# Kernel tuning notes

Measured on AMD Instinct MI355X. Metric: run time of the kernel, lower is better.

Reference implementation:

```python
import jax, jax.numpy as jnp
import numpy as np
import math

DIM = 1024
N_HEADS = 16
HEAD_DIM = DIM // N_HEADS
MAX_LEN = 4096
THETA = 10000.0
LN_EPS = 1e-5


def _rope_tables(dim, max_len, theta=THETA):
    # matches precompute_rope: freqs over even indices, angles = outer(t, freqs)
    inv = 1.0 / theta ** (np.arange(0, dim, 2, dtype=np.float32) / dim)
    t = np.arange(max_len, dtype=np.float32)
    ang = np.outer(t, inv)  # [max_len, dim//2]
    return jnp.asarray(np.cos(ang)), jnp.asarray(np.sin(ang))


def setup_inputs() -> dict:
    key = jax.random.key(0)
    ks = jax.random.split(key, 5)
    B, T, D = 2, 2048, DIM
    s = 1.0 / math.sqrt(D)
    x = jax.random.normal(ks[0], (B, T, D), dtype=jnp.float32)
    wq = jax.random.normal(ks[1], (D, D), dtype=jnp.float32) * s
    wk = jax.random.normal(ks[2], (D, D), dtype=jnp.float32) * s
    wv = jax.random.normal(ks[3], (D, D), dtype=jnp.float32) * s
    wo = jax.random.normal(ks[4], (D, D), dtype=jnp.float32) * s
    ln_g = jnp.ones((D,), dtype=jnp.float32)
    ln_b = jnp.zeros((D,), dtype=jnp.float32)
    cos, sin = _rope_tables(HEAD_DIM, MAX_LEN)
    return {"x": x, "wq": wq, "wk": wk, "wv": wv, "wo": wo,
            "ln_g": ln_g, "ln_b": ln_b, "cos": cos, "sin": sin}


def _rotate(x, cos, sin):
    # x: [B, T, H, hd]; complex multiply on interleaved (even, odd) pairs
    B, T, H, hd = x.shape
    xr = x.reshape(B, T, H, hd // 2, 2)
    x0, x1 = xr[..., 0], xr[..., 1]
    c = cos[None, :T, None, :]
    s = sin[None, :T, None, :]
    o0 = x0 * c - x1 * s
    o1 = x0 * s + x1 * c
    return jnp.stack([o0, o1], axis=-1).reshape(B, T, H, hd)


def reference(x, wq, wk, wv, wo, ln_g, ln_b, cos, sin):
    B, T, D = x.shape
    H, hd = N_HEADS, HEAD_DIM
    # LayerNorm
    mu = jnp.mean(x, axis=-1, keepdims=True)
    var = jnp.var(x, axis=-1, keepdims=True)
    h = (x - mu) * jax.lax.rsqrt(var + LN_EPS) * ln_g + ln_b
    # QKV projections (torch Linear: h @ W.T)
    q = jnp.einsum('btd,ed->bte', h, wq).reshape(B, T, H, hd)
    k = jnp.einsum('btd,ed->bte', h, wk).reshape(B, T, H, hd)
    v = jnp.einsum('btd,ed->bte', h, wv).reshape(B, T, H, hd)
    q = _rotate(q, cos, sin)
    k = _rotate(k, cos, sin)
    # full (non-causal) attention, scores [B, H, T, T]
    scores = jnp.einsum('bqhd,bkhd->bhqk', q, k) / math.sqrt(hd)
    attn = jax.nn.softmax(scores, axis=-1)
    out = jnp.einsum('bhqk,bkhd->bqhd', attn, v).reshape(B, T, D)
    return jnp.einsum('btd,ed->bte', out, wo)
```

## Files before the change

kernel.cpp:

```cpp
#include <hip/hip_runtime.h>
#include <hip/hip_bf16.h>

typedef __attribute__((ext_vector_type(4))) float          fx4;
typedef __attribute__((ext_vector_type(8))) __bf16         bfx8;
typedef __attribute__((ext_vector_type(8))) unsigned short usx8;
typedef __attribute__((ext_vector_type(4))) unsigned short usx4;

#define TLEN 2048
#define ROWS 4096
#define D    1024

__device__ __forceinline__ float bf2f(unsigned short u) {
    union { unsigned int i; float f; } v; v.i = ((unsigned int)u) << 16; return v.f;
}
__device__ __forceinline__ unsigned short f2bf(float f) {
    union { float f; unsigned int i; } v; v.f = f;
    unsigned int r = v.i + 0x7fffu + ((v.i >> 16) & 1u);
    return (unsigned short)(r >> 16);
}
__device__ __forceinline__ unsigned int cvtpk_bf16(float lo, float hi) {
    unsigned int r;
    asm("v_cvt_pk_bf16_f32 %0, %1, %2" : "=v"(r) : "v"(lo), "v"(hi));
    return r;
}
__device__ __forceinline__ float fast_cos(float a) {
    float r; asm("v_cos_f32 %0, %1" : "=v"(r) : "v"(a)); return r;
}
__device__ __forceinline__ float fast_sin(float a) {
    float r; asm("v_sin_f32 %0, %1" : "=v"(r) : "v"(a)); return r;
}
__device__ __forceinline__ void gload_lds16(const unsigned short* g, unsigned short* l) {
    __builtin_amdgcn_global_load_lds((const __attribute__((address_space(1))) void*)g,
                                     (__attribute__((address_space(3))) void*)l, 16, 0, 0);
}

__device__ __forceinline__ usx4 cvt4(fx4 a) {
    usx4 o;
    #pragma unroll
    for (int j = 0; j < 4; j++) o[j] = f2bf(a[j]);
    return o;
}
__global__ __launch_bounds__(256) void prep_kernel(const float* __restrict__ x,
                                                   const float* __restrict__ g,
                                                   const float* __restrict__ bta,
                                                   const float* __restrict__ wq, const float* __restrict__ wk,
                                                   const float* __restrict__ wv, const float* __restrict__ wo,
                                                   unsigned short* __restrict__ hout,
                                                   unsigned short* __restrict__ wqkv,
                                                   unsigned short* __restrict__ wob) {
    const int tid = threadIdx.x;
    if (blockIdx.x >= 4096) {
        const int i = (blockIdx.x - 4096) * 256 + tid;
        ((usx4*)wqkv)[i]          = cvt4(((const fx4*)wq)[i]);
        ((usx4*)wqkv)[262144 + i] = cvt4(((const fx4*)wk)[i]);
        ((usx4*)wqkv)[524288 + i] = cvt4(((const fx4*)wv)[i]);
        ((usx4*)wob)[i]           = cvt4(((const fx4*)wo)[i]);
        return;
    }
    const int row = blockIdx.x;
    fx4 v = ((const fx4*)(x + (size_t)row * D))[tid];
    float s  = v[0] + v[1] + v[2] + v[3];
    float s2 = v[0]*v[0] + v[1]*v[1] + v[2]*v[2] + v[3]*v[3];
    #pragma unroll
    for (int mk = 32; mk >= 1; mk >>= 1) { s += __shfl_xor(s, mk); s2 += __shfl_xor(s2, mk); }
    __shared__ float red[8];
    const int wave = tid >> 6, lane = tid & 63;
    if (lane == 0) { red[wave] = s; red[4 + wave] = s2; }
    __syncthreads();
    s  = red[0] + red[1] + red[2] + red[3];
    s2 = red[4] + red[5] + red[6] + red[7];
    float mu   = s * (1.0f / D);
    float var  = s2 * (1.0f / D) - mu * mu;
    float rstd = rsqrtf(var + 1e-5f);
    fx4 gv = ((const fx4*)g)[tid];
    fx4 bv = ((const fx4*)bta)[tid];
    usx4 o;
    #pragma unroll
    for (int j = 0; j < 4; j++) o[j] = f2bf((v[j] - mu) * rstd * gv[j] + bv[j]);
    ((usx4*)hout)[(size_t)row * 256 + tid] = o;
}

__global__ __launch_bounds__(256) void qkvt_gemm(const unsigned short* __restrict__ hbuf,
                                                 const unsigned short* __restrict__ wqkv,
                                                 unsigned short* __restrict__ qkout,
                                                 unsigned short* __restrict__ vtout) {
    constexpr int K = 1024;
    __shared__ __align__(16) unsigned short As[128 * 64];
    __shared__ __align__(16) unsigned short Bs[128 * 64];
    const int tid = threadIdx.x, lane = tid & 63, wave = tid >> 6;
    const int fr = lane & 15, fq = lane >> 4;
    const int wr = wave >> 1, wc = wave & 1;

    const int id = blockIdx.x;
    const bool isqk = id < 512;
    int bm, bn;
    const unsigned short *Ab, *Bb;
    if (isqk) {
        bm = id & 31; bn = id >> 5;
        Ab = hbuf + (size_t)(bm * 128) * K;
        Bb = wqkv + (size_t)(bn * 128) * K;
    } else {
        int j = id - 512; bm = j & 7; bn = j >> 3;
        Ab = wqkv + (size_t)(2048 * 1024) + (size_t)(bm * 128) * K;
        Bb = hbuf + (size_t)(bn * 128) * K;
    }

    const int srow   = wave * 8 + (lane >> 3);
    const int sc_dst = (lane & 7) * 8;
    const int sc_src = ((lane & 7) ^ (lane >> 3)) * 8;

    fx4 acc[4][4];
    #pragma unroll
    for (int m = 0; m < 4; m++)
        #pragma unroll
        for (int n = 0; n < 4; n++) acc[m][n] = (fx4)0.0f;

    for (int kt = 0; kt < K; kt += 64) {
        #pragma unroll
        for (int i = 0; i < 4; i++) {
            const int r = srow + 32 * i;
            gload_lds16(Ab + (size_t)r * K + kt + sc_src, &As[r * 64 + sc_dst]);
            gload_lds16(Bb + (size_t)r * K + kt + sc_src, &Bs[r * 64 + sc_dst]);
        }
        __syncthreads();
        #pragma unroll
        for (int s = 0; s < 2; s++) {
            bfx8 aF[4], bF[4];
            #pragma unroll
            for (int m = 0; m < 4; m++)
                aF[m] = *(const bfx8*)&As[(wr * 64 + m * 16 + fr) * 64 + (((s * 4 + fq) ^ (fr & 7)) * 8)];
            #pragma unroll
            for (int n = 0; n < 4; n++)
                bF[n] = *(const bfx8*)&Bs[(wc * 64 + n * 16 + fr) * 64 + (((s * 4 + fq) ^ (fr & 7)) * 8)];
            #pragma unroll
            for (int m = 0; m < 4; m++)
                #pragma unroll
                for (int n = 0; n < 4; n++)
                    acc[m][n] = __builtin_amdgcn_mfma_f32_16x16x32_bf16(aF[m], bF[n], acc[m][n], 0, 0, 0);
        }
        __syncthreads();
    }

    const int row0 = bm * 128 + wr * 64 + fq * 4;
    const int col0 = bn * 128 + wc * 64 + fr;
    if (isqk) {
        const float QS = 0.125f * 1.44269504088896f;
        const bool isq = bn < 8;
        const float sgn = (fr & 1) ? 1.0f : -1.0f;
        float fp[4];
        #pragma unroll
        for (int n = 0; n < 4; n++) {
            float pif = (float)(n * 8 + (fr >> 1));
            fp[n] = __builtin_amdgcn_exp2f(fmaf(pif, -0.415241011861f, -2.651496129472f));
        }
        #pragma unroll
        for (int m = 0; m < 4; m++) {
            const int rbase = row0 + m * 16;
            const float tf = (float)(rbase & (TLEN - 1));
            #pragma unroll
            for (int n = 0; n < 4; n++) {
                #pragma unroll
                for (int j = 0; j < 4; j++) {
                    float a = __builtin_amdgcn_fractf((tf + (float)j) * fp[n]);
                    float c = fast_cos(a), s = fast_sin(a);
                    float self = acc[m][n][j];
                    float other = __shfl_xor(self, 1);
                    float o = self * c + other * (sgn * s);
                    if (isq) o *= QS;
                    qkout[(size_t)(rbase + j) * 2048 + col0 + n * 16] = f2bf(o);
                }
            }
        }
    } else {
        const int bb = bn >> 4;
        #pragma unroll
        for (int m = 0; m < 4; m++)
            #pragma unroll
            for (int n = 0; n < 4; n++) {
                const int t = (col0 + n * 16) & (TLEN - 1);
                const int tp = (t & ~63) | ((n >> 1) * 32 + ((fr >> 2)) * 8 + ((n & 1)) * 4 + (fr & 3));
                #pragma unroll
                for (int j = 0; j < 4; j++) {
                    const int d = row0 + m * 16 + j;
                    vtout[(((size_t)(bb * 16 + (d >> 6)) * 64) + (d & 63)) * TLEN + tp] = f2bf(acc[m][n][j]);
                }
            }
    }
}

__global__ __launch_bounds__(256) void gemm_out64(const unsigned short* __restrict__ A,
                                                  const unsigned short* __restrict__ B,
                                                  float* __restrict__ C) {
    constexpr int K = 1024;
    __shared__ __align__(16) unsigned short As[128 * 64];
    __shared__ __align__(16) unsigned short Bs[64 * 64];
    const int tid = threadIdx.x, lane = tid & 63, wave = tid >> 6;
    const int fr = lane & 15, fq = lane >> 4;
    const int bm = blockIdx.x, bn = blockIdx.y;
    const int wr = wave >> 1, wc = wave & 1;

    const int srow   = wave * 8 + (lane >> 3);
    const int sc_dst = (lane & 7) * 8;
    const int sc_src = ((lane & 7) ^ (lane >> 3)) * 8;
    const unsigned short* Ab = A + (size_t)(bm * 128) * K;
    const unsigned short* Bb = B + (size_t)(bn * 64) * K;

    fx4 acc[4][2];
    #pragma unroll
    for (int m = 0; m < 4; m++)
        #pragma unroll
        for (int n = 0; n < 2; n++) acc[m][n] = (fx4)0.0f;

    for (int kt = 0; kt < K; kt += 64) {
        #pragma unroll
        for (int i = 0; i < 4; i++) {
            const int r = srow + 32 * i;
            gload_lds16(Ab + (size_t)r * K + kt + sc_src, &As[r * 64 + sc_dst]);
            if (i < 2)
                gload_lds16(Bb + (size_t)r * K + kt + sc_src, &Bs[r * 64 + sc_dst]);
        }
        __syncthreads();
        #pragma unroll
        for (int s = 0; s < 2; s++) {
            bfx8 aF[4], bF[2];
            #pragma unroll
            for (int m = 0; m < 4; m++)
                aF[m] = *(const bfx8*)&As[(wr * 64 + m * 16 + fr) * 64 + (((s * 4 + fq) ^ (fr & 7)) * 8)];
            #pragma unroll
            for (int n = 0; n < 2; n++)
                bF[n] = *(const bfx8*)&Bs[(wc * 32 + n * 16 + fr) * 64 + (((s * 4 + fq) ^ (fr & 7)) * 8)];
            #pragma unroll
            for (int m = 0; m < 4; m++)
                #pragma unroll
                for (int n = 0; n < 2; n++)
                    acc[m][n] = __builtin_amdgcn_mfma_f32_16x16x32_bf16(aF[m], bF[n], acc[m][n], 0, 0, 0);
        }
        __syncthreads();
    }

    const int row0 = bm * 128 + wr * 64 + fq * 4;
    const int col0 = bn * 64 + wc * 32 + fr;
    #pragma unroll
    for (int m = 0; m < 4; m++)
        #pragma unroll
        for (int n = 0; n < 2; n++)
            #pragma unroll
            for (int j = 0; j < 4; j++)
                C[(size_t)(row0 + m * 16 + j) * 1024 + col0 + n * 16] = acc[m][n][j];
}

__global__ __launch_bounds__(256) void attn_kernel(const unsigned short* __restrict__ qk,
                                                   const unsigned short* __restrict__ vt,
                                                   unsigned short* __restrict__ ao) {
    const int flat = blockIdx.x + (blockIdx.y << 4);
    const int sid  = (flat & 7) * 64 + (flat >> 3);
    const int qt = sid & 15, bh = sid >> 4;
    const int b = bh >> 4, hh = bh & 15;
    const int tid = threadIdx.x, lane = tid & 63, wave = tid >> 6;
    const int fr = lane & 15, fq = lane >> 4;

    __shared__ __align__(16) unsigned short sK[2][64 * 64];
    __shared__ __align__(16) unsigned short sVt[2][64 * 64];

    const size_t rs = 2048;
    const unsigned short* qb  = qk + (size_t)b * TLEN * rs + hh * 64;
    const unsigned short* kb  = qb + 1024;
    const unsigned short* vtb = vt + (size_t)bh * (64 * TLEN);

    bfx8 qF[2][2];
    #pragma unroll
    for (int g = 0; g < 2; g++) {
        int qrow = qt * 128 + g * 64 + wave * 16 + fr;
        const unsigned short* qp = qb + (size_t)qrow * rs + fq * 8;
        qF[g][0] = *(const bfx8*)qp;
        qF[g][1] = *(const bfx8*)(qp + 32);
    }
    union { unsigned short us[8]; bfx8 bf; } ones_u;
    #pragma unroll
    for (int i = 0; i < 8; i++) ones_u.us[i] = 0x3F80;

    const int srow = lane >> 3;
    const int scol = ((lane & 7) ^ srow) * 8;

    #pragma unroll
    for (int i = 0; i < 2; i++) {
        int rg = wave * 2 + i;
        gload_lds16(kb  + (size_t)(rg * 8 + srow) * rs + scol,   &sK[0][rg * 512 + lane * 8]);
        gload_lds16(vtb + (size_t)(rg * 8 + srow) * TLEN + scol, &sVt[0][rg * 512 + lane * 8]);
    }

    fx4 oacc[2][4];
    fx4 oextra[2] = {(fx4)0.0f, (fx4)0.0f};
    #pragma unroll
    for (int g = 0; g < 2; g++)
        #pragma unroll
        for (int db = 0; db < 4; db++) oacc[g][db] = (fx4)0.0f;

    #pragma unroll 2
    for (int t = 0; t < 32; ++t) {
        const int buf = t & 1;
        __syncthreads();

        if (t + 1 < 32) {
            const int kt = (t + 1) * 64;
            #pragma unroll
            for (int i = 0; i < 2; i++) {
                int rg = wave * 2 + i;
                gload_lds16(kb  + (size_t)(kt + rg * 8 + srow) * rs + scol,
                            &sK[buf ^ 1][rg * 512 + lane * 8]);
                gload_lds16(vtb + (size_t)(rg * 8 + srow) * TLEN + kt + scol,
                            &sVt[buf ^ 1][rg * 512 + lane * 8]);
            }
        }

        bfx8 kF[2][4];
        #pragma unroll
        for (int s = 0; s < 2; s++)
            #pragma unroll
            for (int n = 0; n < 4; n++)
                kF[s][n] = *(const bfx8*)&sK[buf][(n * 16 + fr) * 64 + (((s * 4 + fq) ^ (fr & 7)) * 8)];
        fx4 sacc0[4], sacc1[4];
        #pragma unroll
        for (int n = 0; n < 4; n++) { sacc0[n] = (fx4)0.0f; sacc1[n] = (fx4)0.0f; }
        __builtin_amdgcn_s_setprio(1);
        #pragma unroll
        for (int s = 0; s < 2; s++)
            #pragma unroll
            for (int n = 0; n < 4; n++)
                sacc0[n] = __builtin_amdgcn_mfma_f32_16x16x32_bf16(kF[s][n], qF[0][s], sacc0[n], 0, 0, 0);
        #pragma unroll
        for (int s = 0; s < 2; s++)
            #pragma unroll
            for (int n = 0; n < 4; n++)
                sacc1[n] = __builtin_amdgcn_mfma_f32_16x16x32_bf16(kF[s][n], qF[1][s], sacc1[n], 0, 0, 0);
        __builtin_amdgcn_s_setprio(0);

        unsigned int u0[4][2], u1[4][2];
        #pragma unroll
        for (int n = 0; n < 4; n++) {
            u0[n][0] = cvtpk_bf16(__builtin_amdgcn_exp2f(sacc0[n][0]), __builtin_amdgcn_exp2f(sacc0[n][1]));
            u0[n][1] = cvtpk_bf16(__builtin_amdgcn_exp2f(sacc0[n][2]), __builtin_amdgcn_exp2f(sacc0[n][3]));
        }

        bfx8 vF[2][4];
        #pragma unroll
        for (int s = 0; s < 2; s++)
            #pragma unroll
            for (int db = 0; db < 4; db++)
                vF[s][db] = *(const bfx8*)&sVt[buf][(db * 16 + fr) * 64 + (((s * 4 + fq) ^ (fr & 7)) * 8)];

        __builtin_amdgcn_s_setprio(1);
        #pragma unroll
        for (int s = 0; s < 2; s++) {
            union { unsigned int ui[4]; bfx8 bf; } cv;
            cv.ui[0] = u0[2 * s][0];     cv.ui[1] = u0[2 * s][1];
            cv.ui[2] = u0[2 * s + 1][0]; cv.ui[3] = u0[2 * s + 1][1];
            #pragma unroll
            for (int db = 0; db < 4; db++)
                oacc[0][db] = __builtin_amdgcn_mfma_f32_16x16x32_bf16(vF[s][db], cv.bf, oacc[0][db], 0, 0, 0);
            oextra[0] = __builtin_amdgcn_mfma_f32_16x16x32_bf16(ones_u.bf, cv.bf, oextra[0], 0, 0, 0);
        }
        __builtin_amdgcn_s_setprio(0);

        #pragma unroll
        for (int n = 0; n < 4; n++) {
            u1[n][0] = cvtpk_bf16(__builtin_amdgcn_exp2f(sacc1[n][0]), __builtin_amdgcn_exp2f(sacc1[n][1]));
            u1[n][1] = cvtpk_bf16(__builtin_amdgcn_exp2f(sacc1[n][2]), __builtin_amdgcn_exp2f(sacc1[n][3]));
        }

        __builtin_amdgcn_s_setprio(1);
        #pragma unroll
        for (int s = 0; s < 2; s++) {
            union { unsigned int ui[4]; bfx8 bf; } cv;
            cv.ui[0] = u1[2 * s][0];     cv.ui[1] = u1[2 * s][1];
            cv.ui[2] = u1[2 * s + 1][0]; cv.ui[3] = u1[2 * s + 1][1];
            #pragma unroll
            for (int db = 0; db < 4; db++)
                oacc[1][db] = __builtin_amdgcn_mfma_f32_16x16x32_bf16(vF[s][db], cv.bf, oacc[1][db], 0, 0, 0);
            oextra[1] = __builtin_amdgcn_mfma_f32_16x16x32_bf16(ones_u.bf, cv.bf, oextra[1], 0, 0, 0);
        }
        __builtin_amdgcn_s_setprio(0);
    }

    #pragma unroll
    for (int g = 0; g < 2; g++) {
        float invl = 1.0f / oextra[g][0];
        const int qrow = qt * 128 + g * 64 + wave * 16 + fr;
        unsigned short* aop = ao + (size_t)(b * TLEN + qrow) * 1024 + hh * 64 + fq * 4;
        #pragma unroll
        for (int db = 0; db < 4; db++) {
            usx4 o4;
            #pragma unroll
            for (int j = 0; j < 4; j++) o4[j] = f2bf(oacc[g][db][j] * invl);
            *(usx4*)(aop + db * 16) = o4;
        }
    }
}

extern "C" void kernel_launch(void* const* d_in, const int* in_sizes, int n_in,
                              void* d_out, int out_size, void* d_ws, size_t ws_size,
                              hipStream_t stream) {
    const float* x    = (const float*)d_in[0];
    const float* wq   = (const float*)d_in[1];
    const float* wk   = (const float*)d_in[2];
    const float* wv   = (const float*)d_in[3];
    const float* wo   = (const float*)d_in[4];
    const float* lng  = (const float*)d_in[5];
    const float* lnb  = (const float*)d_in[6];

    char* ws = (char*)d_ws;
    unsigned short* wob  = (unsigned short*)(ws);
    unsigned short* wqkv = (unsigned short*)(ws + (2u  << 20));
    unsigned short* hbuf = (unsigned short*)(ws + (8u  << 20));
    unsigned short* qk   = (unsigned short*)(ws + (16u << 20));
    unsigned short* vtb  = (unsigned short*)(ws + (32u << 20));
    unsigned short* ao   = (unsigned short*)(ws + (8u  << 20));

    prep_kernel<<<5120, 256, 0, stream>>>(x, lng, lnb, wq, wk, wv, wo, hbuf, wqkv, wob);
    qkvt_gemm<<<768, 256, 0, stream>>>(hbuf, wqkv, qk, vtb);
    attn_kernel<<<dim3(16, 32), 256, 0, stream>>>(qk, vtb, ao);
    gemm_out64<<<dim3(32, 16), 256, 0, stream>>>(ao, wob, (float*)d_out);
}
```

Before: 117.1 us.

## Precompute RoPE table in prep kernel and widen attention blocks to 512 threads

Two separate changes. First, the prep kernel now fills a cos/sin table using accurate cosf/sinf, stored temporarily in the output buffer. The QKV GEMM epilogue reads this table instead of computing hardware sin/cos with exp2 and fract in the epilogue. Second, the attention kernel now runs 512-thread blocks covering 256 query rows, so each K/V tile staged in LDS serves twice as many queries while each wave issues half as many loads. This trades ALU for extra global reads, and the larger blocks may lower occupancy.

```diff
diff --git a/kernel.cpp b/kernel.cpp
--- a/kernel.cpp
+++ b/kernel.cpp
@@ -22,12 +22,6 @@
     unsigned int r;
     asm("v_cvt_pk_bf16_f32 %0, %1, %2" : "=v"(r) : "v"(lo), "v"(hi));
     return r;
-}
-__device__ __forceinline__ float fast_cos(float a) {
-    float r; asm("v_cos_f32 %0, %1" : "=v"(r) : "v"(a)); return r;
-}
-__device__ __forceinline__ float fast_sin(float a) {
-    float r; asm("v_sin_f32 %0, %1" : "=v"(r) : "v"(a)); return r;
 }
 __device__ __forceinline__ void gload_lds16(const unsigned short* g, unsigned short* l) {
     __builtin_amdgcn_global_load_lds((const __attribute__((address_space(1))) void*)g,
@@ -47,8 +41,18 @@
                                                    const float* __restrict__ wv, const float* __restrict__ wo,
                                                    unsigned short* __restrict__ hout,
                                                    unsigned short* __restrict__ wqkv,
-                                                   unsigned short* __restrict__ wob) {
+                                                   unsigned short* __restrict__ wob,
+                                                   float* __restrict__ ropeTab) {
     const int tid = threadIdx.x;
+    if (blockIdx.x >= 5120) {
+        const int idx = (blockIdx.x - 5120) * 256 + tid;
+        const int pi_ = idx >> 11, t = idx & 2047;
+        float inv = __builtin_amdgcn_exp2f(-0.415241011861f * (float)pi_);
+        float ang = (float)t * inv;
+        ropeTab[idx * 2]     = cosf(ang);
+        ropeTab[idx * 2 + 1] = sinf(ang);
+        return;
+    }
     if (blockIdx.x >= 4096) {
         const int i = (blockIdx.x - 4096) * 256 + tid;
         ((usx4*)wqkv)[i]          = cvt4(((const fx4*)wq)[i]);
@@ -83,7 +87,8 @@
 __global__ __launch_bounds__(256) void qkvt_gemm(const unsigned short* __restrict__ hbuf,
                                                  const unsigned short* __restrict__ wqkv,
                                                  unsigned short* __restrict__ qkout,
-                                                 unsigned short* __restrict__ vtout) {
+                                                 unsigned short* __restrict__ vtout,
+                                                 const float* __restrict__ ropeTab) {
     constexpr int K = 1024;
     __shared__ __align__(16) unsigned short As[128 * 64];
     __shared__ __align__(16) unsigned short Bs[128 * 64];
@@ -147,25 +152,22 @@
         const float QS = 0.125f * 1.44269504088896f;
         const bool isq = bn < 8;
         const float sgn = (fr & 1) ? 1.0f : -1.0f;
-        float fp[4];
-        #pragma unroll
-        for (int n = 0; n < 4; n++) {
-            float pif = (float)(n * 8 + (fr >> 1));
-            fp[n] = __builtin_amdgcn_exp2f(fmaf(pif, -0.415241011861f, -2.651496129472f));
-        }
         #pragma unroll
         for (int m = 0; m < 4; m++) {
             const int rbase = row0 + m * 16;
-            const float tf = (float)(rbase & (TLEN - 1));
+            const int tb = rbase & (TLEN - 1);
             #pragma unroll
             for (int n = 0; n < 4; n++) {
+                const float* tp = ropeTab + ((((n * 8 + (fr >> 1)) << 11) | tb) << 1);
+                fx4 csA = *(const fx4*)tp;
+                fx4 csB = *(const fx4*)(tp + 4);
                 #pragma unroll
                 for (int j = 0; j < 4; j++) {
-                    float a = __builtin_amdgcn_fractf((tf + (float)j) * fp[n]);
-                    float c = fast_cos(a), s = fast_sin(a);
+                    float c  = (j < 2) ? csA[2 * j]     : csB[2 * (j - 2)];
+                    float s_ = (j < 2) ? csA[2 * j + 1] : csB[2 * (j - 2) + 1];
                     float self = acc[m][n][j];
                     float other = __shfl_xor(self, 1);
-                    float o = self * c + other * (sgn * s);
+                    float o = self * c + other * (sgn * s_);
                     if (isq) o *= QS;
                     qkout[(size_t)(rbase + j) * 2048 + col0 + n * 16] = f2bf(o);
                 }
@@ -249,12 +251,12 @@
                 C[(size_t)(row0 + m * 16 + j) * 1024 + col0 + n * 16] = acc[m][n][j];
 }
 
-__global__ __launch_bounds__(256) void attn_kernel(const unsigned short* __restrict__ qk,
+__global__ __launch_bounds__(512) void attn_kernel(const unsigned short* __restrict__ qk,
                                                    const unsigned short* __restrict__ vt,
                                                    unsigned short* __restrict__ ao) {
-    const int flat = blockIdx.x + (blockIdx.y << 4);
-    const int sid  = (flat & 7) * 64 + (flat >> 3);
-    const int qt = sid & 15, bh = sid >> 4;
+    const int flat = blockIdx.x + (blockIdx.y << 3);
+    const int sid  = (flat & 7) * 32 + (flat >> 3);
+    const int qt = sid & 7, bh = sid >> 3;
     const int b = bh >> 4, hh = bh & 15;
     const int tid = threadIdx.x, lane = tid & 63, wave = tid >> 6;
     const int fr = lane & 15, fq = lane >> 4;
@@ -270,7 +272,7 @@
     bfx8 qF[2][2];
     #pragma unroll
     for (int g = 0; g < 2; g++) {
-        int qrow = qt * 128 + g * 64 + wave * 16 + fr;
+        int qrow = qt * 256 + wave * 32 + g * 16 + fr;
         const unsigned short* qp = qb + (size_t)qrow * rs + fq * 8;
         qF[g][0] = *(const bfx8*)qp;
         qF[g][1] = *(const bfx8*)(qp + 32);
@@ -282,12 +284,8 @@
     const int srow = lane >> 3;
     const int scol = ((lane & 7) ^ srow) * 8;
 
-    #pragma unroll
-    for (int i = 0; i < 2; i++) {
-        int rg = wave * 2 + i;
-        gload_lds16(kb  + (size_t)(rg * 8 + srow) * rs + scol,   &sK[0][rg * 512 + lane * 8]);
-        gload_lds16(vtb + (size_t)(rg * 8 + srow) * TLEN + scol, &sVt[0][rg * 512 + lane * 8]);
-    }
+    gload_lds16(kb  + (size_t)(wave * 8 + srow) * rs + scol,   &sK[0][wave * 512 + lane * 8]);
+    gload_lds16(vtb + (size_t)(wave * 8 + srow) * TLEN + scol, &sVt[0][wave * 512 + lane * 8]);
 
     fx4 oacc[2][4];
     fx4 oextra[2] = {(fx4)0.0f, (fx4)0.0f};
@@ -303,14 +301,10 @@
 
         if (t + 1 < 32) {
             const int kt = (t + 1) * 64;
-            #pragma unroll
-            for (int i = 0; i < 2; i++) {
-                int rg = wave * 2 + i;
-                gload_lds16(kb  + (size_t)(kt + rg * 8 + srow) * rs + scol,
-                            &sK[buf ^ 1][rg * 512 + lane * 8]);
-                gload_lds16(vtb + (size_t)(rg * 8 + srow) * TLEN + kt + scol,
-                            &sVt[buf ^ 1][rg * 512 + lane * 8]);
-            }
+            gload_lds16(kb  + (size_t)(kt + wave * 8 + srow) * rs + scol,
+                        &sK[buf ^ 1][wave * 512 + lane * 8]);
+            gload_lds16(vtb + (size_t)(wave * 8 + srow) * TLEN + kt + scol,
+                        &sVt[buf ^ 1][wave * 512 + lane * 8]);
         }
 
         bfx8 kF[2][4];
@@ -385,7 +379,7 @@
     #pragma unroll
     for (int g = 0; g < 2; g++) {
         float invl = 1.0f / oextra[g][0];
-        const int qrow = qt * 128 + g * 64 + wave * 16 + fr;
+        const int qrow = qt * 256 + wave * 32 + g * 16 + fr;
         unsigned short* aop = ao + (size_t)(b * TLEN + qrow) * 1024 + hh * 64 + fq * 4;
         #pragma unroll
         for (int db = 0; db < 4; db++) {
@@ -415,9 +409,10 @@
     unsigned short* qk   = (unsigned short*)(ws + (16u << 20));
     unsigned short* vtb  = (unsigned short*)(ws + (32u << 20));
     unsigned short* ao   = (unsigned short*)(ws + (8u  << 20));
-
-    prep_kernel<<<5120, 256, 0, stream>>>(x, lng, lnb, wq, wk, wv, wo, hbuf, wqkv, wob);
-    qkvt_gemm<<<768, 256, 0, stream>>>(hbuf, wqkv, qk, vtb);
-    attn_kernel<<<dim3(16, 32), 256, 0, stream>>>(qk, vtb, ao);
+    float* ropeTab = (float*)d_out;
+
+    prep_kernel<<<5632, 256, 0, stream>>>(x, lng, lnb, wq, wk, wv, wo, hbuf, wqkv, wob, ropeTab);
+    qkvt_gemm<<<768, 256, 0, stream>>>(hbuf, wqkv, qk, vtb, ropeTab);
+    attn_kernel<<<dim3(8, 32), 512, 0, stream>>>(qk, vtb, ao);
     gemm_out64<<<dim3(32, 16), 256, 0, stream>>>(ao, wob, (float*)d_out);
 }
```

Result: no change. 116.1 us (-0.8%).
